# Kernel optimization log

Hardware: AMD Instinct MI355X
Metric: run time of the kernel (lower is better)

## Reference

```python
import jax, jax.numpy as jnp
import numpy as np

N_NODES = 100000
K = 50000  # ceil(ratio * N) with ratio = nodes_out / nodes_in = 0.5


def setup_inputs() -> dict:
    key = jax.random.key(0)
    k1, k2, k3 = jax.random.split(key, 3)
    x = jax.random.normal(k1, (N_NODES, 256), dtype=jnp.float32)
    edge_index = jax.random.randint(k2, (2, 3200000), 0, N_NODES, dtype=jnp.int64)
    weight = jax.random.normal(k3, (256,), dtype=jnp.float32)
    return {"x": x, "edge_index": edge_index, "weight": weight}


def reference(x, edge_index, weight):
    # --- PyG TopKPooling forward ---
    # score_i = tanh( <x_i, w> / ||w|| )
    score = jnp.tanh((x @ weight) / jnp.linalg.norm(weight))  # [N]
    # select top-k nodes by score
    top_scores, perm = jax.lax.top_k(score, K)  # [K], [K]
    # gather features and gate by score (multiplier)
    x_out = x[perm] * top_scores[:, None]  # [K, C]
    # --- filter_adj: keep edges whose endpoints both survive, remap ids ---
    mapping = jnp.full((x.shape[0],), -1, dtype=edge_index.dtype)
    mapping = mapping.at[perm].set(jnp.arange(K, dtype=edge_index.dtype))
    new_edges = mapping[edge_index]  # [2, E], -1 where endpoint dropped
    valid = (new_edges[0] >= 0) & (new_edges[1] >= 0)
    # fixed-shape output: invalid edges marked -1 (torch returns a compacted
    # variable-length tensor; we keep E fixed for jit-compatibility)
    edge_out = jnp.where(valid[None, :], new_edges, -1)
    return x_out, edge_out
```

## Files before the change

kernel.cpp:

```cpp
#include <hip/hip_runtime.h>
#include <math.h>

#define N_NODES 100000
#define N_FEAT  256
#define K_SEL   50000
#define N_EDGES 3200000
#define NBUCKET 65536

__device__ __forceinline__ unsigned long long descKey(double z) {
    unsigned long long u = (unsigned long long)__double_as_longlong(z);
    unsigned long long a = (u >> 63) ? ~u : (u | 0x8000000000000000ULL);
    return ~a;
}

__device__ __forceinline__ unsigned int bucketOfFloat(float zf) {
    unsigned int u = __float_as_uint(zf);
    unsigned int a = (u >> 31) ? ~u : (u | 0x80000000u);
    return (~a) >> 16;
}

__global__ void norm_kernel(const float* __restrict__ w, double* __restrict__ out) {
    __shared__ double sd[256];
    int t = threadIdx.x;
    double v = (double)w[t];
    sd[t] = v * v;
    __syncthreads();
    for (int off = 128; off > 0; off >>= 1) {
        if (t < off) sd[t] += sd[t + off];
        __syncthreads();
    }
    if (t == 0) out[0] = sqrt(sd[0]);
}

__global__ void score_kernel(const float* __restrict__ x, const float* __restrict__ w,
                             const double* __restrict__ normp,
                             unsigned long long* __restrict__ key64,
                             int* __restrict__ bucket, float* __restrict__ score,
                             int* __restrict__ hist) {
    int row  = (int)((blockIdx.x * blockDim.x + threadIdx.x) >> 6);
    int lane = threadIdx.x & 63;
    if (row >= N_NODES) return;
    const float4 xv = ((const float4*)(x + (size_t)row * N_FEAT))[lane];
    const float4 wv = ((const float4*)w)[lane];
    double acc = (double)xv.x * (double)wv.x + (double)xv.y * (double)wv.y +
                 (double)xv.z * (double)wv.z + (double)xv.w * (double)wv.w;
    for (int m = 32; m >= 1; m >>= 1) acc += __shfl_xor(acc, m, 64);
    if (lane == 0) {
        double z = acc / normp[0];
        key64[row] = descKey(z);
        int b = (int)bucketOfFloat((float)z);
        bucket[row] = b;
        score[row] = (float)tanh(z);
        atomicAdd(&hist[b], 1);
    }
}

__global__ void __launch_bounds__(1024) scan_kernel(const int* __restrict__ hist,
                                                    int* __restrict__ start) {
    __shared__ int sums[1024];
    int t = threadIdx.x;
    int base = t * 64;
    int s = 0;
    for (int j = 0; j < 64; ++j) { start[base + j] = s; s += hist[base + j]; }
    sums[t] = s;
    __syncthreads();
    for (int off = 1; off < 1024; off <<= 1) {
        int v = (t >= off) ? sums[t - off] : 0;
        __syncthreads();
        sums[t] += v;
        __syncthreads();
    }
    int pre = (t == 0) ? 0 : sums[t - 1];
    for (int j = 0; j < 64; ++j) start[base + j] += pre;
}

__global__ void scatter_kernel(const unsigned long long* __restrict__ key64,
                               const int* __restrict__ bucket,
                               const int* __restrict__ start, int* __restrict__ cursor,
                               unsigned long long* __restrict__ slotKey,
                               int* __restrict__ slotIdx) {
    int i = blockIdx.x * blockDim.x + threadIdx.x;
    if (i >= N_NODES) return;
    int b = bucket[i];
    int pos = start[b] + atomicAdd(&cursor[b], 1);
    slotKey[pos] = key64[i];
    slotIdx[pos] = i;
}

__global__ void rank_kernel(const unsigned long long* __restrict__ slotKey,
                            const int* __restrict__ slotIdx,
                            const int* __restrict__ bucket,
                            const int* __restrict__ start, const int* __restrict__ hist,
                            const float* __restrict__ score,
                            int* __restrict__ mapping, int* __restrict__ perm,
                            float* __restrict__ selScore) {
    int s = blockIdx.x * blockDim.x + threadIdx.x;
    if (s >= N_NODES) return;
    int i = slotIdx[s];
    int b = bucket[i];
    unsigned long long myKey = slotKey[s];
    int st = start[b], cnt = hist[b];
    int rank = 0;
    for (int t = st; t < st + cnt; ++t) {
        unsigned long long k = slotKey[t];
        if (k < myKey || (k == myKey && slotIdx[t] < i)) ++rank;
    }
    int p = st + rank;
    if (p < K_SEL) {
        mapping[i] = p;
        perm[p] = i;
        selScore[p] = score[i];
    } else {
        mapping[i] = -1;
    }
}

__global__ void gather_kernel(const float* __restrict__ x, const int* __restrict__ perm,
                              const float* __restrict__ selScore, float* __restrict__ out) {
    int tid = blockIdx.x * blockDim.x + threadIdx.x;
    int r = tid >> 6;
    if (r >= K_SEL) return;
    int c = (tid & 63) << 2;
    int src = perm[r];
    float sc = selScore[r];
    float4 v = *(const float4*)(x + (size_t)src * N_FEAT + c);
    float4 o;
    o.x = v.x * sc; o.y = v.y * sc; o.z = v.z * sc; o.w = v.w * sc;
    *(float4*)(out + (size_t)r * N_FEAT + c) = o;
}

__global__ void edge_kernel(const int* __restrict__ ei, const int* __restrict__ mapping,
                            float* __restrict__ out) {
    int e = blockIdx.x * blockDim.x + threadIdx.x;
    if (e >= N_EDGES) return;
    int a = ei[e];
    int b = ei[e + N_EDGES];
    int ma = mapping[a];
    int mb = mapping[b];
    bool valid = (ma >= 0) && (mb >= 0);
    out[e]           = valid ? (float)ma : -1.0f;
    out[e + N_EDGES] = valid ? (float)mb : -1.0f;
}

extern "C" void kernel_launch(void* const* d_in, const int* in_sizes, int n_in,
                              void* d_out, int out_size, void* d_ws, size_t ws_size,
                              hipStream_t stream) {
    const float* x  = (const float*)d_in[0];
    const int*   ei = (const int*)d_in[1];
    const float* w  = (const float*)d_in[2];
    float* out = (float*)d_out;

    char* p = (char*)d_ws;
    double* d_norm = (double*)p;                 p += 16;
    unsigned long long* key64   = (unsigned long long*)p; p += (size_t)N_NODES * 8;
    unsigned long long* slotKey = (unsigned long long*)p; p += (size_t)N_NODES * 8;
    float* score  = (float*)p;  p += (size_t)N_NODES * 4;
    int*   bucket = (int*)p;    p += (size_t)N_NODES * 4;
    int*   mapping= (int*)p;    p += (size_t)N_NODES * 4;
    int*   slotIdx= (int*)p;    p += (size_t)N_NODES * 4;
    int*   perm   = (int*)p;    p += (size_t)K_SEL * 4;
    float* selScore=(float*)p;  p += (size_t)K_SEL * 4;
    int*   hist   = (int*)p;    p += (size_t)NBUCKET * 4;
    int*   cursor = (int*)p;    p += (size_t)NBUCKET * 4;
    int*   start  = (int*)p;    p += (size_t)NBUCKET * 4;

    hipMemsetAsync(hist, 0, (size_t)NBUCKET * 4 * 2, stream);

    norm_kernel<<<1, 256, 0, stream>>>(w, d_norm);

    int waves_blocks = (N_NODES * 64 + 255) / 256;
    score_kernel<<<waves_blocks, 256, 0, stream>>>(x, w, d_norm, key64, bucket, score, hist);

    scan_kernel<<<1, 1024, 0, stream>>>(hist, start);

    int node_blocks = (N_NODES + 255) / 256;
    scatter_kernel<<<node_blocks, 256, 0, stream>>>(key64, bucket, start, cursor,
                                                    slotKey, slotIdx);

    rank_kernel<<<node_blocks, 256, 0, stream>>>(slotKey, slotIdx, bucket, start, hist,
                                                 score, mapping, perm, selScore);

    gather_kernel<<<(K_SEL * 64) / 256, 256, 0, stream>>>(x, perm, selScore, out);

    edge_kernel<<<(N_EDGES + 255) / 256, 256, 0, stream>>>(ei, mapping,
                                                           out + (size_t)K_SEL * N_FEAT);
}
```

Measured before the change: 348.3 us.

## Fuse gather and edge kernels, drop norm division from scoring, vectorize scan

Sorting now runs on the raw dot product rather than dot/norm, which is valid because the norm is positive and the ordering is unchanged. The norm and tanh are applied only to the selected rows inside a new fused output kernel that handles both the feature gather and the edge remapping, with the edge part processing four edges per thread through int4 loads. The memset is replaced by an init kernel that also computes the norm. The separate cursor array is dropped by advancing start in place with atomics, the scan uses int4 loads and stores, and the bucket and score arrays are recomputed on the fly. This saves launches and memory traffic, but tanhf in float and bucketing on the float dot rather than the scaled value could change near-tie ordering relative to the reference.

Result: faster. 319.6 us, median of 2 (-8.2%).

```diff
diff --git a/kernel.cpp b/kernel.cpp
--- a/kernel.cpp
+++ b/kernel.cpp
@@ -7,6 +7,9 @@
 #define N_EDGES 3200000
 #define NBUCKET 65536
 
+#define GATHER_BLOCKS (K_SEL / 4)
+#define EDGE_BLOCKS   (N_EDGES / (4 * 256))
+
 __device__ __forceinline__ unsigned long long descKey(double z) {
     unsigned long long u = (unsigned long long)__double_as_longlong(z);
     unsigned long long a = (u >> 63) ? ~u : (u | 0x8000000000000000ULL);
@@ -19,24 +22,27 @@
     return (~a) >> 16;
 }
 
-__global__ void norm_kernel(const float* __restrict__ w, double* __restrict__ out) {
+__global__ void init_kernel(const float* __restrict__ w, double* __restrict__ norm,
+                            int* __restrict__ hist) {
     __shared__ double sd[256];
-    int t = threadIdx.x;
-    double v = (double)w[t];
-    sd[t] = v * v;
-    __syncthreads();
-    for (int off = 128; off > 0; off >>= 1) {
-        if (t < off) sd[t] += sd[t + off];
+    int t = blockIdx.x * blockDim.x + threadIdx.x;
+    hist[t] = 0;
+    if (blockIdx.x == 0) {
+        int tt = threadIdx.x;
+        double v = (double)w[tt];
+        sd[tt] = v * v;
         __syncthreads();
-    }
-    if (t == 0) out[0] = sqrt(sd[0]);
+        for (int off = 128; off > 0; off >>= 1) {
+            if (tt < off) sd[tt] += sd[tt + off];
+            __syncthreads();
+        }
+        if (tt == 0) norm[0] = sqrt(sd[0]);
+    }
 }
 
 __global__ void score_kernel(const float* __restrict__ x, const float* __restrict__ w,
-                             const double* __restrict__ normp,
                              unsigned long long* __restrict__ key64,
-                             int* __restrict__ bucket, float* __restrict__ score,
-                             int* __restrict__ hist) {
+                             float* __restrict__ dotf, int* __restrict__ hist) {
     int row  = (int)((blockIdx.x * blockDim.x + threadIdx.x) >> 6);
     int lane = threadIdx.x & 63;
     if (row >= N_NODES) return;
@@ -46,62 +52,74 @@
                  (double)xv.z * (double)wv.z + (double)xv.w * (double)wv.w;
     for (int m = 32; m >= 1; m >>= 1) acc += __shfl_xor(acc, m, 64);
     if (lane == 0) {
-        double z = acc / normp[0];
-        key64[row] = descKey(z);
-        int b = (int)bucketOfFloat((float)z);
-        bucket[row] = b;
-        score[row] = (float)tanh(z);
-        atomicAdd(&hist[b], 1);
-    }
-}
-
-__global__ void __launch_bounds__(1024) scan_kernel(const int* __restrict__ hist,
+        key64[row] = descKey(acc);
+        float df = (float)acc;
+        dotf[row] = df;
+        atomicAdd(&hist[bucketOfFloat(df)], 1);
+    }
+}
+
+__global__ void __launch_bounds__(1024) scan_kernel(const int4* __restrict__ hist4,
                                                     int* __restrict__ start) {
     __shared__ int sums[1024];
     int t = threadIdx.x;
-    int base = t * 64;
+    int4 v[16];
+#pragma unroll
+    for (int j = 0; j < 16; ++j) v[j] = hist4[t * 16 + j];
     int s = 0;
-    for (int j = 0; j < 64; ++j) { start[base + j] = s; s += hist[base + j]; }
+#pragma unroll
+    for (int j = 0; j < 16; ++j) { s += v[j].x + v[j].y + v[j].z + v[j].w; }
     sums[t] = s;
     __syncthreads();
     for (int off = 1; off < 1024; off <<= 1) {
-        int v = (t >= off) ? sums[t - off] : 0;
+        int vv = (t >= off) ? sums[t - off] : 0;
         __syncthreads();
-        sums[t] += v;
+        sums[t] += vv;
         __syncthreads();
     }
-    int pre = (t == 0) ? 0 : sums[t - 1];
-    for (int j = 0; j < 64; ++j) start[base + j] += pre;
+    int run = (t == 0) ? 0 : sums[t - 1];
+    int4* start4 = (int4*)start;
+#pragma unroll
+    for (int j = 0; j < 16; ++j) {
+        int4 o;
+        o.x = run; run += v[j].x;
+        o.y = run; run += v[j].y;
+        o.z = run; run += v[j].z;
+        o.w = run; run += v[j].w;
+        start4[t * 16 + j] = o;
+    }
 }
 
 __global__ void scatter_kernel(const unsigned long long* __restrict__ key64,
-                               const int* __restrict__ bucket,
-                               const int* __restrict__ start, int* __restrict__ cursor,
+                               const float* __restrict__ dotf,
+                               int* __restrict__ start,
                                unsigned long long* __restrict__ slotKey,
                                int* __restrict__ slotIdx) {
     int i = blockIdx.x * blockDim.x + threadIdx.x;
     if (i >= N_NODES) return;
-    int b = bucket[i];
-    int pos = start[b] + atomicAdd(&cursor[b], 1);
+    int b = (int)bucketOfFloat(dotf[i]);
+    int pos = atomicAdd(&start[b], 1);
     slotKey[pos] = key64[i];
     slotIdx[pos] = i;
 }
 
 __global__ void rank_kernel(const unsigned long long* __restrict__ slotKey,
                             const int* __restrict__ slotIdx,
-                            const int* __restrict__ bucket,
                             const int* __restrict__ start, const int* __restrict__ hist,
-                            const float* __restrict__ score,
+                            const float* __restrict__ dotf,
                             int* __restrict__ mapping, int* __restrict__ perm,
-                            float* __restrict__ selScore) {
+                            float* __restrict__ selDot) {
     int s = blockIdx.x * blockDim.x + threadIdx.x;
     if (s >= N_NODES) return;
+    unsigned long long myKey = slotKey[s];
     int i = slotIdx[s];
-    int b = bucket[i];
-    unsigned long long myKey = slotKey[s];
-    int st = start[b], cnt = hist[b];
+    float df = dotf[i];
+    int b = (int)bucketOfFloat(df);
+    int end = start[b];
+    int cnt = hist[b];
+    int st = end - cnt;
     int rank = 0;
-    for (int t = st; t < st + cnt; ++t) {
+    for (int t = st; t < end; ++t) {
         unsigned long long k = slotKey[t];
         if (k < myKey || (k == myKey && slotIdx[t] < i)) ++rank;
     }
@@ -109,37 +127,48 @@
     if (p < K_SEL) {
         mapping[i] = p;
         perm[p] = i;
-        selScore[p] = score[i];
+        selDot[p] = df;
     } else {
         mapping[i] = -1;
     }
 }
 
-__global__ void gather_kernel(const float* __restrict__ x, const int* __restrict__ perm,
-                              const float* __restrict__ selScore, float* __restrict__ out) {
-    int tid = blockIdx.x * blockDim.x + threadIdx.x;
-    int r = tid >> 6;
-    if (r >= K_SEL) return;
-    int c = (tid & 63) << 2;
-    int src = perm[r];
-    float sc = selScore[r];
-    float4 v = *(const float4*)(x + (size_t)src * N_FEAT + c);
-    float4 o;
-    o.x = v.x * sc; o.y = v.y * sc; o.z = v.z * sc; o.w = v.w * sc;
-    *(float4*)(out + (size_t)r * N_FEAT + c) = o;
-}
-
-__global__ void edge_kernel(const int* __restrict__ ei, const int* __restrict__ mapping,
-                            float* __restrict__ out) {
-    int e = blockIdx.x * blockDim.x + threadIdx.x;
-    if (e >= N_EDGES) return;
-    int a = ei[e];
-    int b = ei[e + N_EDGES];
-    int ma = mapping[a];
-    int mb = mapping[b];
-    bool valid = (ma >= 0) && (mb >= 0);
-    out[e]           = valid ? (float)ma : -1.0f;
-    out[e + N_EDGES] = valid ? (float)mb : -1.0f;
+__global__ void out_kernel(const float* __restrict__ x, const int* __restrict__ perm,
+                           const float* __restrict__ selDot,
+                           const double* __restrict__ normp,
+                           const int* __restrict__ ei, const int* __restrict__ mapping,
+                           float* __restrict__ out) {
+    if (blockIdx.x < GATHER_BLOCKS) {
+        int tid = blockIdx.x * 256 + threadIdx.x;
+        int r = tid >> 6;
+        int c = (tid & 63) << 2;
+        int src = perm[r];
+        float sc = tanhf(selDot[r] / (float)normp[0]);
+        float4 v = *(const float4*)(x + (size_t)src * N_FEAT + c);
+        float4 o;
+        o.x = v.x * sc; o.y = v.y * sc; o.z = v.z * sc; o.w = v.w * sc;
+        *(float4*)(out + (size_t)r * N_FEAT + c) = o;
+    } else {
+        int tid = (blockIdx.x - GATHER_BLOCKS) * 256 + threadIdx.x;
+        int e = tid << 2;
+        int4 a = *(const int4*)(ei + e);
+        int4 b = *(const int4*)(ei + N_EDGES + e);
+        float* oeu = out + (size_t)K_SEL * N_FEAT;
+        float* oev = oeu + N_EDGES;
+        int m0 = mapping[a.x], m1 = mapping[a.y], m2 = mapping[a.z], m3 = mapping[a.w];
+        int n0 = mapping[b.x], n1 = mapping[b.y], n2 = mapping[b.z], n3 = mapping[b.w];
+        float4 ou, ov;
+        bool v0 = (m0 >= 0) && (n0 >= 0);
+        bool v1 = (m1 >= 0) && (n1 >= 0);
+        bool v2 = (m2 >= 0) && (n2 >= 0);
+        bool v3 = (m3 >= 0) && (n3 >= 0);
+        ou.x = v0 ? (float)m0 : -1.0f; ov.x = v0 ? (float)n0 : -1.0f;
+        ou.y = v1 ? (float)m1 : -1.0f; ov.y = v1 ? (float)n1 : -1.0f;
+        ou.z = v2 ? (float)m2 : -1.0f; ov.z = v2 ? (float)n2 : -1.0f;
+        ou.w = v3 ? (float)m3 : -1.0f; ov.w = v3 ? (float)n3 : -1.0f;
+        *(float4*)(oeu + e) = ou;
+        *(float4*)(oev + e) = ov;
+    }
 }
 
 extern "C" void kernel_launch(void* const* d_in, const int* in_sizes, int n_in,
@@ -151,37 +180,30 @@
     float* out = (float*)d_out;
 
     char* p = (char*)d_ws;
-    double* d_norm = (double*)p;                 p += 16;
+    double* d_norm = (double*)p;                          p += 16;
     unsigned long long* key64   = (unsigned long long*)p; p += (size_t)N_NODES * 8;
     unsigned long long* slotKey = (unsigned long long*)p; p += (size_t)N_NODES * 8;
-    float* score  = (float*)p;  p += (size_t)N_NODES * 4;
-    int*   bucket = (int*)p;    p += (size_t)N_NODES * 4;
+    float* dotf   = (float*)p;  p += (size_t)N_NODES * 4;
     int*   mapping= (int*)p;    p += (size_t)N_NODES * 4;
     int*   slotIdx= (int*)p;    p += (size_t)N_NODES * 4;
     int*   perm   = (int*)p;    p += (size_t)K_SEL * 4;
-    float* selScore=(float*)p;  p += (size_t)K_SEL * 4;
+    float* selDot = (float*)p;  p += (size_t)K_SEL * 4;
     int*   hist   = (int*)p;    p += (size_t)NBUCKET * 4;
-    int*   cursor = (int*)p;    p += (size_t)NBUCKET * 4;
     int*   start  = (int*)p;    p += (size_t)NBUCKET * 4;
 
-    hipMemsetAsync(hist, 0, (size_t)NBUCKET * 4 * 2, stream);
-
-    norm_kernel<<<1, 256, 0, stream>>>(w, d_norm);
+    init_kernel<<<NBUCKET / 256, 256, 0, stream>>>(w, d_norm, hist);
 
     int waves_blocks = (N_NODES * 64 + 255) / 256;
-    score_kernel<<<waves_blocks, 256, 0, stream>>>(x, w, d_norm, key64, bucket, score, hist);
-
-    scan_kernel<<<1, 1024, 0, stream>>>(hist, start);
+    score_kernel<<<waves_blocks, 256, 0, stream>>>(x, w, key64, dotf, hist);
+
+    scan_kernel<<<1, 1024, 0, stream>>>((const int4*)hist, start);
 
     int node_blocks = (N_NODES + 255) / 256;
-    scatter_kernel<<<node_blocks, 256, 0, stream>>>(key64, bucket, start, cursor,
-                                                    slotKey, slotIdx);
-
-    rank_kernel<<<node_blocks, 256, 0, stream>>>(slotKey, slotIdx, bucket, start, hist,
-                                                 score, mapping, perm, selScore);
-
-    gather_kernel<<<(K_SEL * 64) / 256, 256, 0, stream>>>(x, perm, selScore, out);
-
-    edge_kernel<<<(N_EDGES + 255) / 256, 256, 0, stream>>>(ei, mapping,
-                                                           out + (size_t)K_SEL * N_FEAT);
-}
+    scatter_kernel<<<node_blocks, 256, 0, stream>>>(key64, dotf, start, slotKey, slotIdx);
+
+    rank_kernel<<<node_blocks, 256, 0, stream>>>(slotKey, slotIdx, start, hist, dotf,
+                                                 mapping, perm, selDot);
+
+    out_kernel<<<GATHER_BLOCKS + EDGE_BLOCKS, 256, 0, stream>>>(x, perm, selDot, d_norm,
+                                                                ei, mapping, out);
+}
```
